# Kernel optimization log

Measured on AMD Instinct MI355X. Metric: run time of the kernel, lower is better.

## Reference

```python
import jax, jax.numpy as jnp
import numpy as np

N = 50000
E = 800000
D_IN = 128
D_HID = 128
N_CLASSES = 40


def setup_inputs() -> dict:
    key = jax.random.key(0)
    ks = jax.random.split(key, 8)
    features = jax.random.normal(ks[0], (N, D_IN), dtype=jnp.float32)
    src = jax.random.randint(ks[1], (E,), 0, N)
    dst = jax.random.randint(ks[2], (E,), 0, N)
    edge_index = jnp.stack([src, dst]).astype(jnp.int64)
    def glorot(k, fan_in, fan_out):
        return jax.random.normal(k, (fan_in, fan_out), dtype=jnp.float32) * (1.0 / np.sqrt(fan_in))
    W1 = glorot(ks[3], D_IN, D_HID)
    W2 = glorot(ks[4], D_HID, D_HID)
    W3 = glorot(ks[5], D_HID, N_CLASSES)
    return {
        "features": features,
        "edge_index": edge_index,
        "W1": W1, "b1": jnp.zeros((D_HID,), jnp.float32),
        "W2": W2, "b2": jnp.zeros((D_HID,), jnp.float32),
        "W3": W3, "b3": jnp.zeros((N_CLASSES,), jnp.float32),
    }


def reference(features, edge_index, W1, b1, W2, b2, W3, b3):
    # DGL GraphConv with norm='both': h = D_out^{-1/2} A^T D_in^{-1/2} ... i.e.
    # out[v] = deg_in(v)^{-1/2} * sum_{(u->v) in E} deg_out(u)^{-1/2} * x[u], then @ W + b
    src, dst = edge_index[0], edge_index[1]
    n = features.shape[0]
    ones = jnp.ones((src.shape[0],), features.dtype)
    deg_out = jnp.maximum(jax.ops.segment_sum(ones, src, num_segments=n), 1.0)
    deg_in = jnp.maximum(jax.ops.segment_sum(ones, dst, num_segments=n), 1.0)
    norm_src = deg_out ** -0.5  # [N]
    norm_dst = deg_in ** -0.5   # [N]

    def conv(x, W, b):
        msg = (x * norm_src[:, None])[src]                      # [E, d] gather
        agg = jax.ops.segment_sum(msg, dst, num_segments=n)     # [N, d] scatter-add
        return (agg * norm_dst[:, None]) @ W + b

    # bns=False default -> BatchNorm skipped; dropout p=0.0 -> identity
    h = jax.nn.relu(conv(features, W1, b1))
    h = jax.nn.relu(conv(h, W2, b2))
    return conv(h, W3, b3)  # [N, n_classes]
```

## Files before the change

kernel.cpp:

```cpp
#include <hip/hip_runtime.h>


#define EPB 4096
#define SCAN_CHUNK 4096

typedef short v8s __attribute__((ext_vector_type(8)));
typedef float v4f __attribute__((ext_vector_type(4)));

__device__ __forceinline__ ushort f2bf(float f) {
    unsigned u = __float_as_uint(f);
    unsigned r = (u + 0x7fffu + ((u >> 16) & 1u)) >> 16;
    return (ushort)r;
}
__device__ __forceinline__ void unpack2(unsigned w, float& lo, float& hi) {
    lo = __uint_as_float(w << 16);
    hi = __uint_as_float(w & 0xffff0000u);
}

__global__ __launch_bounds__(256) void front_kernel(const int* __restrict__ ei, int E,
        int nblk1, int NB, int* __restrict__ hist_all,
        ushort* __restrict__ rankD, ushort* __restrict__ rankS,
        const float* __restrict__ W1, const float* __restrict__ W2,
        const float* __restrict__ W3,
        ushort* __restrict__ W1f, ushort* __restrict__ W2f, ushort* __restrict__ W3f) {
    __shared__ int hd[512];
    __shared__ int hs[512];
    int t = threadIdx.x;
    if ((int)blockIdx.x >= nblk1) {
        int idx = ((int)blockIdx.x - nblk1) * 256 + t;
        const float* W; ushort* Wf; int Dout, NF, base;
        if (idx < 2048)      { W = W1; Wf = W1f; Dout = 128; NF = 8; base = idx; }
        else if (idx < 4096) { W = W2; Wf = W2f; Dout = 128; NF = 8; base = idx - 2048; }
        else if (idx < 5120) { W = W3; Wf = W3f; Dout = 40;  NF = 4; base = idx - 4096; }
        else return;
        int lane = base & 63;
        int f = (base >> 6) % NF;
        int ks = base / (64 * NF);
        int c = f * 16 + (lane & 15);
        int kbase = ks * 32 + (lane >> 4) * 8;
        unsigned p[4];
        #pragma unroll
        for (int j = 0; j < 4; ++j) {
            float wlo = (c < Dout) ? W[(size_t)(kbase + 2 * j) * Dout + c] : 0.f;
            float whi = (c < Dout) ? W[(size_t)(kbase + 2 * j + 1) * Dout + c] : 0.f;
            p[j] = (unsigned)f2bf(wlo) | ((unsigned)f2bf(whi) << 16);
        }
        *reinterpret_cast<uint4*>(Wf + (size_t)base * 8) = make_uint4(p[0], p[1], p[2], p[3]);
        return;
    }
    int blk = blockIdx.x;
    for (int i = t; i < 512; i += 256) { hd[i] = 0; hs[i] = 0; }
    __syncthreads();
    int base = blk * EPB;
    #pragma unroll
    for (int j = 0; j < 16; ++j) {
        int e = base + j * 256 + t;
        if (e < E) {
            int s = ei[e], d = ei[E + e];
            rankS[e] = (ushort)atomicAdd(&hs[s >> 8], 1);
            rankD[e] = (ushort)atomicAdd(&hd[d >> 8], 1);
        }
    }
    __syncthreads();
    int L = NB * nblk1;
    for (int b = t; b < NB; b += 256) {
        hist_all[b * nblk1 + blk]     = hd[b];
        hist_all[L + b * nblk1 + blk] = hs[b];
    }
}

__global__ __launch_bounds__(256) void scanA_kernel(const int* __restrict__ data, int L2,
                                                    int* __restrict__ partials) {
    __shared__ int red[256];
    int t = threadIdx.x;
    int base = blockIdx.x * SCAN_CHUNK;
    int s = 0;
    for (int i = t; i < SCAN_CHUNK; i += 256) {
        int idx = base + i;
        if (idx < L2) s += data[idx];
    }
    red[t] = s;
    __syncthreads();
    for (int off = 128; off > 0; off >>= 1) {
        if (t < off) red[t] += red[t + off];
        __syncthreads();
    }
    if (t == 0) partials[blockIdx.x] = red[0];
}

__global__ __launch_bounds__(256) void scanB_kernel(int* __restrict__ partials, int nparts) {
    __shared__ int s[256];
    int t = threadIdx.x;
    s[t] = (t < nparts) ? partials[t] : 0;
    __syncthreads();
    for (int off = 1; off < 256; off <<= 1) {
        int v = (t >= off) ? s[t - off] : 0;
        __syncthreads();
        s[t] += v;
        __syncthreads();
    }
    if (t < nparts) partials[t] = s[t] - partials[t];
}

__global__ __launch_bounds__(256) void scanC_kernel(int* __restrict__ data, int L2,
                                                    const int* __restrict__ partials) {
    __shared__ int tsum[256];
    int t = threadIdx.x;
    int base = blockIdx.x * SCAN_CHUNK + t * 16;
    int local[16];
    int s = 0;
    #pragma unroll
    for (int i = 0; i < 16; ++i) {
        int idx = base + i;
        int v = (idx < L2) ? data[idx] : 0;
        local[i] = v;
        s += v;
    }
    tsum[t] = s;
    __syncthreads();
    for (int off = 1; off < 256; off <<= 1) {
        int v = (t >= off) ? tsum[t - off] : 0;
        __syncthreads();
        tsum[t] += v;
        __syncthreads();
    }
    int run = partials[blockIdx.x] + (t ? tsum[t - 1] : 0);
    #pragma unroll
    for (int i = 0; i < 16; ++i) {
        int idx = base + i;
        if (idx < L2) {
            data[idx] = run;
            run += local[i];
        }
    }
}

template<int NF, int DO_NS, int FP32IN>
__device__ __forceinline__ void mm_body(const void* __restrict__ Xv,
        const ushort* __restrict__ Wf, const float* __restrict__ ns,
        ushort* __restrict__ out, int n, int blk, int wv, int lane) {
    int row0 = (blk * 4 + wv) * 16;
    if (row0 >= n) return;
    int arow = row0 + (lane & 15);
    if (arow >= n) arow = n - 1;
    int kgrp = lane >> 4;
    const v8s* bp = reinterpret_cast<const v8s*>(Wf);
    v4f acc[NF];
    #pragma unroll
    for (int f = 0; f < NF; ++f) acc[f] = (v4f){0.f, 0.f, 0.f, 0.f};
    #pragma unroll
    for (int ks = 0; ks < 4; ++ks) {
        v8s a;
        if (FP32IN) {
            const float* xp = (const float*)Xv + (size_t)arow * 128 + (ks * 4 + kgrp) * 8;
            float4 lo = *reinterpret_cast<const float4*>(xp);
            float4 hi = *reinterpret_cast<const float4*>(xp + 4);
            a[0] = (short)f2bf(lo.x); a[1] = (short)f2bf(lo.y);
            a[2] = (short)f2bf(lo.z); a[3] = (short)f2bf(lo.w);
            a[4] = (short)f2bf(hi.x); a[5] = (short)f2bf(hi.y);
            a[6] = (short)f2bf(hi.z); a[7] = (short)f2bf(hi.w);
        } else {
            const v8s* ap = reinterpret_cast<const v8s*>((const ushort*)Xv + (size_t)arow * 128);
            a = ap[ks * 4 + kgrp];
        }
        #pragma unroll
        for (int f = 0; f < NF; ++f) {
            v8s b = bp[(ks * NF + f) * 64 + lane];
            acc[f] = __builtin_amdgcn_mfma_f32_16x16x32_bf16(a, b, acc[f], 0, 0, 0);
        }
    }
    int rbase = row0 + (lane >> 4) * 4;
    int ccol = lane & 15;
    constexpr int OS = NF * 16;
    #pragma unroll
    for (int r = 0; r < 4; ++r) {
        int gr = rbase + r;
        if (gr < n) {
            float s = DO_NS ? ns[gr] : 1.f;
            #pragma unroll
            for (int f = 0; f < NF; ++f)
                out[(size_t)gr * OS + f * 16 + ccol] = f2bf(s * acc[f][r]);
        }
    }
}

__global__ __launch_bounds__(256) void scatter_mm1_kernel(const int* __restrict__ ei, int E,
        int nblk1, int NB, const int* __restrict__ hist_all,
        const ushort* __restrict__ rankD, const ushort* __restrict__ rankS,
        unsigned* __restrict__ packD, unsigned char* __restrict__ srcb,
        const float* __restrict__ features, const ushort* __restrict__ W1f,
        ushort* __restrict__ xb, int n) {
    int t = threadIdx.x;
    if ((int)blockIdx.x >= nblk1) {
        int blk = (int)blockIdx.x - nblk1;
        mm_body<8, 0, 1>(features, W1f, nullptr, xb, n, blk, t >> 6, t & 63);
        return;
    }
    int blk = blockIdx.x;
    int base = blk * EPB;
    int L = NB * nblk1;
    #pragma unroll
    for (int j = 0; j < 16; ++j) {
        int e = base + j * 256 + t;
        if (e < E) {
            int s = ei[e], d = ei[E + e];
            int posD = hist_all[(d >> 8) * nblk1 + blk] + (int)rankD[e];
            packD[posD] = ((unsigned)(d & 255) << 24) | (unsigned)s;
            int posS = hist_all[L + (s >> 8) * nblk1 + blk] - E + (int)rankS[e];
            srcb[posS] = (unsigned char)(s & 255);
        }
    }
}

__global__ __launch_bounds__(256) void bucket_kernel(const unsigned* __restrict__ packD,
        const unsigned char* __restrict__ srcb, const int* __restrict__ hist_all,
        int nblk1, int NB, int n, int E,
        int* __restrict__ row_ptr, int* __restrict__ col,
        float* __restrict__ norm_src, float* __restrict__ norm_dst) {
    int t = threadIdx.x;
    __shared__ int cnt[256];
    __shared__ int incl[256];
    __shared__ int cur[256];
    if ((int)blockIdx.x < NB) {
        int B = blockIdx.x;
        int s0 = hist_all[B * nblk1];
        int s1 = (B + 1 < NB) ? hist_all[(B + 1) * nblk1] : E;
        cnt[t] = 0;
        __syncthreads();
        for (int i = s0 + t; i < s1; i += 256)
            atomicAdd(&cnt[packD[i] >> 24], 1);
        __syncthreads();
        int v = cnt[t];
        incl[t] = v;
        __syncthreads();
        for (int off = 1; off < 256; off <<= 1) {
            int w = (t >= off) ? incl[t - off] : 0;
            __syncthreads();
            incl[t] += w;
            __syncthreads();
        }
        int excl = incl[t] - v;
        cur[t] = excl;
        int node = B * 256 + t;
        if (node < n) {
            row_ptr[node] = s0 + excl;
            norm_dst[node] = rsqrtf((float)(v > 0 ? v : 1));
        }
        if (B == NB - 1 && t == 0) row_ptr[n] = E;
        __syncthreads();
        for (int i = s0 + t; i < s1; i += 256) {
            unsigned p = packD[i];
            int r = atomicAdd(&cur[p >> 24], 1);
            col[s0 + r] = (int)(p & 0xFFFFFFu);
        }
    } else {
        int B = (int)blockIdx.x - NB;
        int L = NB * nblk1;
        int s0 = hist_all[L + B * nblk1] - E;
        int s1 = (B + 1 < NB) ? (hist_all[L + (B + 1) * nblk1] - E) : E;
        cnt[t] = 0;
        __syncthreads();
        for (int i = s0 + t; i < s1; i += 256)
            atomicAdd(&cnt[srcb[i]], 1);
        __syncthreads();
        int node = B * 256 + t;
        if (node < n) {
            int v = cnt[t];
            norm_src[node] = rsqrtf((float)(v > 0 ? v : 1));
        }
    }
}

template<int NF, int DO_NS>
__global__ __launch_bounds__(256) void mm_mfma_kernel(const ushort* __restrict__ X,
        const ushort* __restrict__ Wf, const float* __restrict__ ns,
        ushort* __restrict__ out, int n) {
    int t = threadIdx.x;
    mm_body<NF, DO_NS, 0>(X, Wf, ns, out, n, (int)blockIdx.x, t >> 6, t & 63);
}

template<int EDGE_NS, int MODE_NS>
__global__ __launch_bounds__(256) void agg128_kernel(const ushort* __restrict__ xb,
        const int* __restrict__ row_ptr, const int* __restrict__ col,
        const float* __restrict__ bias, const float* __restrict__ norm_dst,
        const float* __restrict__ norm_src, ushort* __restrict__ out, int n) {
    int wid  = (blockIdx.x * blockDim.x + threadIdx.x) >> 6;
    int lane = threadIdx.x & 63;
    if (wid >= n) return;
    int start = row_ptr[wid], end = row_ptr[wid + 1];
    int quarter = lane >> 4, l4 = lane & 15;
    float acc[8];
    #pragma unroll
    for (int i = 0; i < 8; ++i) acc[i] = 0.f;
    for (int b = start; b < end; b += 64) {
        int m = end - b; if (m > 64) m = 64;
        int u = 0; float s = 1.f;
        if (lane < m) {
            u = col[b + lane];
            if (EDGE_NS) s = norm_src[u];
        }
        for (int j = 0; j < m; j += 4) {
            int jj = j + quarter;
            int uu = __shfl(u, jj);
            float ss = EDGE_NS ? __shfl(s, jj) : 1.f;
            if (jj < m) {
                const uint4 v = *reinterpret_cast<const uint4*>(xb + (size_t)uu * 128 + 8 * l4);
                float f0, f1;
                if (EDGE_NS) {
                    unpack2(v.x, f0, f1); acc[0] = fmaf(ss, f0, acc[0]); acc[1] = fmaf(ss, f1, acc[1]);
                    unpack2(v.y, f0, f1); acc[2] = fmaf(ss, f0, acc[2]); acc[3] = fmaf(ss, f1, acc[3]);
                    unpack2(v.z, f0, f1); acc[4] = fmaf(ss, f0, acc[4]); acc[5] = fmaf(ss, f1, acc[5]);
                    unpack2(v.w, f0, f1); acc[6] = fmaf(ss, f0, acc[6]); acc[7] = fmaf(ss, f1, acc[7]);
                } else {
                    unpack2(v.x, f0, f1); acc[0] += f0; acc[1] += f1;
                    unpack2(v.y, f0, f1); acc[2] += f0; acc[3] += f1;
                    unpack2(v.z, f0, f1); acc[4] += f0; acc[5] += f1;
                    unpack2(v.w, f0, f1); acc[6] += f0; acc[7] += f1;
                }
            }
        }
    }
    #pragma unroll
    for (int i = 0; i < 8; ++i) {
        acc[i] += __shfl_xor(acc[i], 16);
        acc[i] += __shfl_xor(acc[i], 32);
    }
    if (lane < 16) {
        float nd = norm_dst[wid];
        float sc = MODE_NS ? norm_src[wid] : 1.f;
        const float* bp = bias + 8 * lane;
        unsigned p[4];
        #pragma unroll
        for (int i = 0; i < 4; ++i) {
            float lo = fmaxf(fmaf(nd, acc[2 * i],     bp[2 * i]),     0.f) * sc;
            float hi = fmaxf(fmaf(nd, acc[2 * i + 1], bp[2 * i + 1]), 0.f) * sc;
            p[i] = (unsigned)f2bf(lo) | ((unsigned)f2bf(hi) << 16);
        }
        *reinterpret_cast<uint4*>(out + (size_t)wid * 128 + 8 * lane) =
            make_uint4(p[0], p[1], p[2], p[3]);
    }
}

__global__ __launch_bounds__(256) void agg40_kernel(const ushort* __restrict__ yb,
        const int* __restrict__ row_ptr, const int* __restrict__ col,
        const float* __restrict__ norm_dst, const float* __restrict__ b3,
        float* __restrict__ out, int n) {
    int wid  = (blockIdx.x * blockDim.x + threadIdx.x) >> 6;
    int lane = threadIdx.x & 63;
    if (wid >= n) return;
    int start = row_ptr[wid], end = row_ptr[wid + 1];
    int oct = lane >> 3, l8 = lane & 7;
    float acc[8];
    #pragma unroll
    for (int i = 0; i < 8; ++i) acc[i] = 0.f;
    for (int b = start; b < end; b += 64) {
        int m = end - b; if (m > 64) m = 64;
        int u = 0;
        if (lane < m) u = col[b + lane];
        for (int j = 0; j < m; j += 8) {
            int jj = j + oct;
            int uu = __shfl(u, jj);
            if (jj < m) {
                const uint4 v = *reinterpret_cast<const uint4*>(yb + (size_t)uu * 64 + 8 * l8);
                float f0, f1;
                unpack2(v.x, f0, f1); acc[0] += f0; acc[1] += f1;
                unpack2(v.y, f0, f1); acc[2] += f0; acc[3] += f1;
                unpack2(v.z, f0, f1); acc[4] += f0; acc[5] += f1;
                unpack2(v.w, f0, f1); acc[6] += f0; acc[7] += f1;
            }
        }
    }
    #pragma unroll
    for (int i = 0; i < 8; ++i) {
        acc[i] += __shfl_xor(acc[i], 8);
        acc[i] += __shfl_xor(acc[i], 16);
        acc[i] += __shfl_xor(acc[i], 32);
    }
    if (lane < 5) {
        float nd = norm_dst[wid];
        const float* bp = b3 + 8 * lane;
        float* op = out + (size_t)wid * 40 + 8 * lane;
        float4 o0, o1;
        o0.x = fmaf(nd, acc[0], bp[0]); o0.y = fmaf(nd, acc[1], bp[1]);
        o0.z = fmaf(nd, acc[2], bp[2]); o0.w = fmaf(nd, acc[3], bp[3]);
        o1.x = fmaf(nd, acc[4], bp[4]); o1.y = fmaf(nd, acc[5], bp[5]);
        o1.z = fmaf(nd, acc[6], bp[6]); o1.w = fmaf(nd, acc[7], bp[7]);
        *reinterpret_cast<float4*>(op)     = o0;
        *reinterpret_cast<float4*>(op + 4) = o1;
    }
}

extern "C" void kernel_launch(void* const* d_in, const int* in_sizes, int n_in,
                              void* d_out, int out_size, void* d_ws, size_t ws_size,
                              hipStream_t stream) {
    const float* features = (const float*)d_in[0];
    const int*   ei       = (const int*)d_in[1];
    const float* W1 = (const float*)d_in[2];
    const float* b1 = (const float*)d_in[3];
    const float* W2 = (const float*)d_in[4];
    const float* b2 = (const float*)d_in[5];
    const float* W3 = (const float*)d_in[6];
    const float* b3 = (const float*)d_in[7];

    const int n = in_sizes[0] / 128;
    const int E = in_sizes[1] / 2;

    const int nblk1 = (E + EPB - 1) / EPB;
    const int NB    = (n + 255) >> 8;
    const int L     = NB * nblk1;
    const int L2    = 2 * L;
    const int sb2   = (L2 + SCAN_CHUNK - 1) / SCAN_CHUNK;

    char* w = (char*)d_ws;
    auto alloc = [&](size_t bytes) {
        char* p = w;
        w += (bytes + 255) & ~(size_t)255;
        return p;
    };
    int*    hist_all = (int*)   alloc((size_t)L2 * 4);
    int*    partials = (int*)   alloc((size_t)256 * 4);
    float*  norm_src = (float*) alloc((size_t)n * 4);
    float*  norm_dst = (float*) alloc((size_t)n * 4);
    int*    row_ptr  = (int*)   alloc((size_t)(n + 1) * 4);
    int*    col      = (int*)   alloc((size_t)E * 4);
    ushort* xb       = (ushort*)alloc((size_t)n * 128 * 2);
    ushort* hb       = (ushort*)alloc((size_t)n * 128 * 2);
    ushort* W1f      = (ushort*)alloc((size_t)16384 * 2);
    ushort* W2f      = (ushort*)alloc((size_t)16384 * 2);
    ushort* W3f      = (ushort*)alloc((size_t)8192 * 2);

    char* scr = (char*)hb;
    ushort*        rankD = (ushort*)scr;                 scr += ((size_t)E * 2 + 255) & ~(size_t)255;
    ushort*        rankS = (ushort*)scr;                 scr += ((size_t)E * 2 + 255) & ~(size_t)255;
    unsigned*      packD = (unsigned*)scr;               scr += ((size_t)E * 4 + 255) & ~(size_t)255;
    unsigned char* srcb  = (unsigned char*)scr;
    ushort* yb = xb;

    int mmb = (n + 63) / 64;
    int ab  = (n + 3) / 4;

    front_kernel<<<nblk1 + 20, 256, 0, stream>>>(ei, E, nblk1, NB, hist_all,
                                                 rankD, rankS, W1, W2, W3, W1f, W2f, W3f);
    scanA_kernel<<<sb2, 256, 0, stream>>>(hist_all, L2, partials);
    scanB_kernel<<<1, 256, 0, stream>>>(partials, sb2);
    scanC_kernel<<<sb2, 256, 0, stream>>>(hist_all, L2, partials);
    scatter_mm1_kernel<<<nblk1 + mmb, 256, 0, stream>>>(ei, E, nblk1, NB, hist_all,
                                                        rankD, rankS, packD, srcb,
                                                        features, W1f, xb, n);
    bucket_kernel<<<2 * NB, 256, 0, stream>>>(packD, srcb, hist_all, nblk1, NB, n, E,
                                              row_ptr, col, norm_src, norm_dst);
    agg128_kernel<1, 0><<<ab, 256, 0, stream>>>(xb, row_ptr, col, b1, norm_dst,
                                                norm_src, hb, n);
    mm_mfma_kernel<8, 1><<<mmb, 256, 0, stream>>>(hb, W2f, norm_src, xb, n);
    agg128_kernel<0, 1><<<ab, 256, 0, stream>>>(xb, row_ptr, col, b2, norm_dst,
                                                norm_src, hb, n);
    mm_mfma_kernel<4, 0><<<mmb, 256, 0, stream>>>(hb, W3f, nullptr, yb, n);
    agg40_kernel<<<ab, 256, 0, stream>>>(yb, row_ptr, col, norm_dst, b3, (float*)d_out, n);
}
```

Before: 178.5 us.

## Fuse neighbor aggregation with following MFMA matmul in one kernel per layer

Replaces the separate agg128 and mm_mfma kernels with a fused aggmm kernel. Each block aggregates 16 destination rows into shared memory as bf16, then multiplies them by the next layer's weights with MFMA and writes the projected result directly. This removes the intermediate hidden-state round trip through global memory and two kernel launches. In exchange, each block handles fewer rows for the matmul, re-reads the weights per block, and adds a separate scratch allocation so the aggregation temporaries no longer alias the feature buffer.

```diff
diff --git a/kernel.cpp b/kernel.cpp
--- a/kernel.cpp
+++ b/kernel.cpp
@@ -271,73 +271,108 @@
     }
 }
 
-template<int NF, int DO_NS>
-__global__ __launch_bounds__(256) void mm_mfma_kernel(const ushort* __restrict__ X,
-        const ushort* __restrict__ Wf, const float* __restrict__ ns,
-        ushort* __restrict__ out, int n) {
-    int t = threadIdx.x;
-    mm_body<NF, DO_NS, 0>(X, Wf, ns, out, n, (int)blockIdx.x, t >> 6, t & 63);
-}
-
-template<int EDGE_NS, int MODE_NS>
-__global__ __launch_bounds__(256) void agg128_kernel(const ushort* __restrict__ xb,
+template<int EDGE_NS, int ACT_NS, int NF_TOT, int MM_NS, int PAD40>
+__global__ __launch_bounds__(256) void aggmm_kernel(const ushort* __restrict__ xt,
         const int* __restrict__ row_ptr, const int* __restrict__ col,
         const float* __restrict__ bias, const float* __restrict__ norm_dst,
-        const float* __restrict__ norm_src, ushort* __restrict__ out, int n) {
-    int wid  = (blockIdx.x * blockDim.x + threadIdx.x) >> 6;
-    int lane = threadIdx.x & 63;
-    if (wid >= n) return;
-    int start = row_ptr[wid], end = row_ptr[wid + 1];
+        const float* __restrict__ norm_src, const ushort* __restrict__ Wf,
+        ushort* __restrict__ out, int n) {
+    __shared__ ushort Xl[16][136];
+    int t = threadIdx.x;
+    int wv = t >> 6, lane = t & 63;
+    int row0 = (int)blockIdx.x * 16;
     int quarter = lane >> 4, l4 = lane & 15;
-    float acc[8];
-    #pragma unroll
-    for (int i = 0; i < 8; ++i) acc[i] = 0.f;
-    for (int b = start; b < end; b += 64) {
-        int m = end - b; if (m > 64) m = 64;
-        int u = 0; float s = 1.f;
-        if (lane < m) {
-            u = col[b + lane];
-            if (EDGE_NS) s = norm_src[u];
-        }
-        for (int j = 0; j < m; j += 4) {
-            int jj = j + quarter;
-            int uu = __shfl(u, jj);
-            float ss = EDGE_NS ? __shfl(s, jj) : 1.f;
-            if (jj < m) {
-                const uint4 v = *reinterpret_cast<const uint4*>(xb + (size_t)uu * 128 + 8 * l4);
-                float f0, f1;
-                if (EDGE_NS) {
-                    unpack2(v.x, f0, f1); acc[0] = fmaf(ss, f0, acc[0]); acc[1] = fmaf(ss, f1, acc[1]);
-                    unpack2(v.y, f0, f1); acc[2] = fmaf(ss, f0, acc[2]); acc[3] = fmaf(ss, f1, acc[3]);
-                    unpack2(v.z, f0, f1); acc[4] = fmaf(ss, f0, acc[4]); acc[5] = fmaf(ss, f1, acc[5]);
-                    unpack2(v.w, f0, f1); acc[6] = fmaf(ss, f0, acc[6]); acc[7] = fmaf(ss, f1, acc[7]);
-                } else {
-                    unpack2(v.x, f0, f1); acc[0] += f0; acc[1] += f1;
-                    unpack2(v.y, f0, f1); acc[2] += f0; acc[3] += f1;
-                    unpack2(v.z, f0, f1); acc[4] += f0; acc[5] += f1;
-                    unpack2(v.w, f0, f1); acc[6] += f0; acc[7] += f1;
+    for (int i = 0; i < 4; ++i) {
+        int vi = row0 + wv * 4 + i;
+        int lrow = wv * 4 + i;
+        if (vi < n) {
+            int start = row_ptr[vi], end = row_ptr[vi + 1];
+            float acc[8];
+            #pragma unroll
+            for (int q = 0; q < 8; ++q) acc[q] = 0.f;
+            for (int b = start; b < end; b += 64) {
+                int m = end - b; if (m > 64) m = 64;
+                int u = 0; float s = 1.f;
+                if (lane < m) {
+                    u = col[b + lane];
+                    if (EDGE_NS) s = norm_src[u];
+                }
+                for (int j = 0; j < m; j += 4) {
+                    int jj = j + quarter;
+                    int uu = __shfl(u, jj);
+                    float ss = EDGE_NS ? __shfl(s, jj) : 1.f;
+                    if (jj < m) {
+                        const uint4 v = *reinterpret_cast<const uint4*>(xt + (size_t)uu * 128 + 8 * l4);
+                        float f0, f1;
+                        if (EDGE_NS) {
+                            unpack2(v.x, f0, f1); acc[0] = fmaf(ss, f0, acc[0]); acc[1] = fmaf(ss, f1, acc[1]);
+                            unpack2(v.y, f0, f1); acc[2] = fmaf(ss, f0, acc[2]); acc[3] = fmaf(ss, f1, acc[3]);
+                            unpack2(v.z, f0, f1); acc[4] = fmaf(ss, f0, acc[4]); acc[5] = fmaf(ss, f1, acc[5]);
+                            unpack2(v.w, f0, f1); acc[6] = fmaf(ss, f0, acc[6]); acc[7] = fmaf(ss, f1, acc[7]);
+                        } else {
+                            unpack2(v.x, f0, f1); acc[0] += f0; acc[1] += f1;
+                            unpack2(v.y, f0, f1); acc[2] += f0; acc[3] += f1;
+                            unpack2(v.z, f0, f1); acc[4] += f0; acc[5] += f1;
+                            unpack2(v.w, f0, f1); acc[6] += f0; acc[7] += f1;
+                        }
+                    }
                 }
             }
-        }
-    }
-    #pragma unroll
-    for (int i = 0; i < 8; ++i) {
-        acc[i] += __shfl_xor(acc[i], 16);
-        acc[i] += __shfl_xor(acc[i], 32);
-    }
-    if (lane < 16) {
-        float nd = norm_dst[wid];
-        float sc = MODE_NS ? norm_src[wid] : 1.f;
-        const float* bp = bias + 8 * lane;
-        unsigned p[4];
+            #pragma unroll
+            for (int q = 0; q < 8; ++q) {
+                acc[q] += __shfl_xor(acc[q], 16);
+                acc[q] += __shfl_xor(acc[q], 32);
+            }
+            if (lane < 16) {
+                float nd = norm_dst[vi];
+                float sc = ACT_NS ? norm_src[vi] : 1.f;
+                const float* bp = bias + 8 * lane;
+                unsigned p[4];
+                #pragma unroll
+                for (int q = 0; q < 4; ++q) {
+                    float lo = fmaxf(fmaf(nd, acc[2 * q],     bp[2 * q]),     0.f) * sc;
+                    float hi = fmaxf(fmaf(nd, acc[2 * q + 1], bp[2 * q + 1]), 0.f) * sc;
+                    p[q] = (unsigned)f2bf(lo) | ((unsigned)f2bf(hi) << 16);
+                }
+                *reinterpret_cast<uint4*>(&Xl[lrow][8 * lane]) = make_uint4(p[0], p[1], p[2], p[3]);
+            }
+        } else if (lane < 16) {
+            *reinterpret_cast<uint4*>(&Xl[lrow][8 * lane]) = make_uint4(0, 0, 0, 0);
+        }
+    }
+    __syncthreads();
+    constexpr int FPW = NF_TOT / 4;
+    const v8s* bp = reinterpret_cast<const v8s*>(Wf);
+    int kgrp = lane >> 4;
+    v4f acc[FPW];
+    #pragma unroll
+    for (int f = 0; f < FPW; ++f) acc[f] = (v4f){0.f, 0.f, 0.f, 0.f};
+    #pragma unroll
+    for (int ks = 0; ks < 4; ++ks) {
+        v8s a = *reinterpret_cast<const v8s*>(&Xl[lane & 15][(ks * 4 + kgrp) * 8]);
         #pragma unroll
-        for (int i = 0; i < 4; ++i) {
-            float lo = fmaxf(fmaf(nd, acc[2 * i],     bp[2 * i]),     0.f) * sc;
-            float hi = fmaxf(fmaf(nd, acc[2 * i + 1], bp[2 * i + 1]), 0.f) * sc;
-            p[i] = (unsigned)f2bf(lo) | ((unsigned)f2bf(hi) << 16);
-        }
-        *reinterpret_cast<uint4*>(out + (size_t)wid * 128 + 8 * lane) =
-            make_uint4(p[0], p[1], p[2], p[3]);
+        for (int f = 0; f < FPW; ++f) {
+            int F = wv * FPW + f;
+            v8s b = bp[(ks * NF_TOT + F) * 64 + lane];
+            acc[f] = __builtin_amdgcn_mfma_f32_16x16x32_bf16(a, b, acc[f], 0, 0, 0);
+        }
+    }
+    int rbase = row0 + (lane >> 4) * 4;
+    int ccol = lane & 15;
+    constexpr int OS = NF_TOT * 16;
+    #pragma unroll
+    for (int r = 0; r < 4; ++r) {
+        int gr = rbase + r;
+        if (gr < n) {
+            float s = MM_NS ? norm_src[gr] : 1.f;
+            #pragma unroll
+            for (int f = 0; f < FPW; ++f) {
+                int colo = (wv * FPW + f) * 16 + ccol;
+                ushort val = f2bf(s * acc[f][r]);
+                if (PAD40 && colo >= 40) val = 0;
+                out[(size_t)gr * OS + colo] = val;
+            }
+        }
     }
 }
 
@@ -423,20 +458,22 @@
     float*  norm_dst = (float*) alloc((size_t)n * 4);
     int*    row_ptr  = (int*)   alloc((size_t)(n + 1) * 4);
     int*    col      = (int*)   alloc((size_t)E * 4);
-    ushort* xb       = (ushort*)alloc((size_t)n * 128 * 2);
-    ushort* hb       = (ushort*)alloc((size_t)n * 128 * 2);
+    ushort* xb1      = (ushort*)alloc((size_t)n * 128 * 2);
+    ushort* xb2      = (ushort*)alloc((size_t)n * 128 * 2);
+    char*   scratch  = (char*)  alloc((size_t)12 * E);
     ushort* W1f      = (ushort*)alloc((size_t)16384 * 2);
     ushort* W2f      = (ushort*)alloc((size_t)16384 * 2);
     ushort* W3f      = (ushort*)alloc((size_t)8192 * 2);
 
-    char* scr = (char*)hb;
+    char* scr = scratch;
     ushort*        rankD = (ushort*)scr;                 scr += ((size_t)E * 2 + 255) & ~(size_t)255;
     ushort*        rankS = (ushort*)scr;                 scr += ((size_t)E * 2 + 255) & ~(size_t)255;
     unsigned*      packD = (unsigned*)scr;               scr += ((size_t)E * 4 + 255) & ~(size_t)255;
     unsigned char* srcb  = (unsigned char*)scr;
-    ushort* yb = xb;
+    ushort* yb = (ushort*)scratch;
 
     int mmb = (n + 63) / 64;
+    int fb  = (n + 15) / 16;
     int ab  = (n + 3) / 4;
 
     front_kernel<<<nblk1 + 20, 256, 0, stream>>>(ei, E, nblk1, NB, hist_all,
@@ -446,14 +483,12 @@
     scanC_kernel<<<sb2, 256, 0, stream>>>(hist_all, L2, partials);
     scatter_mm1_kernel<<<nblk1 + mmb, 256, 0, stream>>>(ei, E, nblk1, NB, hist_all,
                                                         rankD, rankS, packD, srcb,
-                                                        features, W1f, xb, n);
+                                                        features, W1f, xb1, n);
     bucket_kernel<<<2 * NB, 256, 0, stream>>>(packD, srcb, hist_all, nblk1, NB, n, E,
                                               row_ptr, col, norm_src, norm_dst);
-    agg128_kernel<1, 0><<<ab, 256, 0, stream>>>(xb, row_ptr, col, b1, norm_dst,
-                                                norm_src, hb, n);
-    mm_mfma_kernel<8, 1><<<mmb, 256, 0, stream>>>(hb, W2f, norm_src, xb, n);
-    agg128_kernel<0, 1><<<ab, 256, 0, stream>>>(xb, row_ptr, col, b2, norm_dst,
-                                                norm_src, hb, n);
-    mm_mfma_kernel<4, 0><<<mmb, 256, 0, stream>>>(hb, W3f, nullptr, yb, n);
+    aggmm_kernel<1, 0, 8, 1, 0><<<fb, 256, 0, stream>>>(xb1, row_ptr, col, b1,
+                                                        norm_dst, norm_src, W2f, xb2, n);
+    aggmm_kernel<0, 1, 4, 0, 1><<<fb, 256, 0, stream>>>(xb2, row_ptr, col, b2,
+                                                        norm_dst, norm_src, W3f, yb, n);
     agg40_kernel<<<ab, 256, 0, stream>>>(yb, row_ptr, col, norm_dst, b3, (float*)d_out, n);
 }
```

Result: faster. 164.1 us (-8.1%).
